# Kernel optimization log

Hardware: AMD Instinct MI355X
Metric: run time of the kernel (lower is better)

Reference implementation:

```python
import jax, jax.numpy as jnp
import numpy as np

N_ENTITY = 100000
D = 128          # entity_hidden_size = hidden_size // 2
HID = 256        # hidden_size
N_REL = 48
N_BASES = 8
N_EDGES = 1000000
B_SZ, E_LEN = 32, 32


def setup_inputs() -> dict:
    key = jax.random.key(0)
    ks = jax.random.split(key, 12)
    s = 0.05
    return {
        "node_embeds": jax.random.normal(ks[0], (N_ENTITY, D), jnp.float32) * s,
        "bases": jax.random.normal(ks[1], (N_BASES, D, D), jnp.float32) * s,
        "comp": jax.random.normal(ks[2], (N_REL, N_BASES), jnp.float32) * s,
        "root": jax.random.normal(ks[3], (D, D), jnp.float32) * s,
        "bias": jnp.zeros((D,), jnp.float32),
        "w1": jax.random.normal(ks[4], (D, D // 2), jnp.float32) * s,
        "b1": jnp.zeros((D // 2,), jnp.float32),
        "w2": jax.random.normal(ks[5], (D // 2, D), jnp.float32) * s,
        "b2": jnp.zeros((D,), jnp.float32),
        "wp": jax.random.normal(ks[6], (D, HID), jnp.float32) * s,
        "bp": jnp.zeros((HID,), jnp.float32),
        "edge_index": jax.random.randint(ks[7], (2, N_EDGES), 0, N_ENTITY, dtype=jnp.int32),
        "edge_type": jax.random.randint(ks[8], (N_EDGES,), 0, N_REL, dtype=jnp.int32),
        "entity_ids": jax.random.randint(ks[9], (B_SZ, E_LEN), 0, N_ENTITY, dtype=jnp.int32),
    }


def _rgcn(x, bases, comp, root, bias, edge_index, edge_type):
    # PyG RGCNConv with basis decomposition, aggr='mean' per (node, relation).
    n = x.shape[0]
    r, b = comp.shape
    src, dst = edge_index[0], edge_index[1]
    # per-(target, relation) in-degree for mean normalization
    seg = dst * r + edge_type                                   # [E]
    deg = jax.ops.segment_sum(jnp.ones_like(edge_type, jnp.float32), seg, num_segments=n * r)
    norm = 1.0 / jnp.maximum(deg, 1.0)
    c = comp[edge_type] * norm[seg][:, None]                    # [E, B] relation coeffs * norm
    x_src = x[src]                                              # [E, D] gather
    out = x @ root + bias                                       # root transform
    for k in range(b):                                          # small fixed basis loop
        agg = jax.ops.segment_sum(c[:, k:k + 1] * x_src, dst, num_segments=n)  # [N, D]
        out = out + agg @ bases[k]
    return out


def reference(node_embeds, bases, comp, root, bias, w1, b1, w2, b2, wp, bp,
              edge_index, edge_type, entity_ids):
    h = _rgcn(node_embeds, bases, comp, root, bias, edge_index, edge_type) + node_embeds
    h = (jax.nn.relu(h @ w1 + b1) @ w2 + b2) + h                # entity_proj1 + residual
    ent = h @ wp + bp                                           # entity_proj2 -> [N, HID]
    return ent[entity_ids]                                      # [B, L, HID]
```

## Files before the change

### kernel.cpp

```cpp
#include <hip/hip_runtime.h>

#define N_ENTITY 100000
#define D 128
#define HID 256
#define N_REL 48
#define N_BASES 8
#define N_EDGES 1000000
#define NPOS 1024
#define ECAP 96

#define OFF_MAP    0
#define OFF_BITMAP 100032
#define OFF_UCNT   103232
#define OFF_BKT    104256
#define OFF_ENT    202560

__global__ void k_register(const int* __restrict__ eids, int* __restrict__ map,
                           unsigned int* __restrict__ bitmap, int* __restrict__ ucnt) {
    int tid = threadIdx.x;
    for (int i = tid; i < 3200; i += 1024) bitmap[i] = 0u;
    ucnt[tid] = 0;
    __syncthreads();
    int e = eids[tid];
    atomicMin(&map[e], tid);
    atomicOr(&bitmap[e >> 5], 1u << (e & 31));
}

__global__ __launch_bounds__(256) void k_count(
        const int* __restrict__ src, const int* __restrict__ dst,
        const int* __restrict__ etype, const int* __restrict__ map,
        const unsigned int* __restrict__ bitmap, int* __restrict__ ucnt,
        int* __restrict__ bkt) {
    int base = (blockIdx.x * 256 + threadIdx.x) * 4;
    if (base >= N_EDGES) return;
    const int4 d4 = *reinterpret_cast<const int4*>(dst + base);
    #pragma unroll
    for (int q = 0; q < 4; ++q) {
        int d = (&d4.x)[q];
        if ((bitmap[d >> 5] >> (d & 31)) & 1u) {
            int e = base + q;
            int u = map[d];
            int pos = atomicAdd(&ucnt[u], 1);
            if (pos < ECAP)
                bkt[u * ECAP + pos] = src[e] | (etype[e] << 17);
        }
    }
}

__global__ __launch_bounds__(512) void k_fused2(
        const int* __restrict__ eids, const int* __restrict__ ucnt,
        const int* __restrict__ bkt, const float* __restrict__ x,
        const float* __restrict__ comp, const float* __restrict__ bases,
        const float* __restrict__ root, const float* __restrict__ bias,
        const float* __restrict__ w1, const float* __restrict__ b1,
        const float* __restrict__ w2, const float* __restrict__ b2,
        const float* __restrict__ wp, const float* __restrict__ bp,
        float* __restrict__ ent) {
    __shared__ float xs[2][D];
    __shared__ float accs[2][N_BASES * D];
    __shared__ float hs[2][D];
    __shared__ float t1s[2][D / 2];
    __shared__ float h2s[2][D];
    __shared__ float part[4096];
    __shared__ float ctab[ECAP][N_BASES];
    __shared__ int esrc[ECAP], eti[ECAP];
    __shared__ int deg48[N_REL];
    __shared__ int enames[2];

    int tid = threadIdx.x;
    int u0 = blockIdx.x * 2;
    if (tid < 2) enames[tid] = eids[u0 + tid];
    __syncthreads();
    if (tid < 256) {
        int s = tid >> 7, dd = tid & 127;
        xs[s][dd] = x[(size_t)enames[s] * D + dd];
    }

    {
        int d = tid & 127;
        int kg = tid >> 7;
        for (int s = 0; s < 2; ++s) {
            int u = u0 + s;
            int n = ucnt[u]; if (n > ECAP) n = ECAP;
            if (tid < N_REL) deg48[tid] = 0;
            if (tid < n) {
                int w = bkt[u * ECAP + tid];
                esrc[tid] = w & 0x1FFFF;
                eti[tid] = w >> 17;
            }
            __syncthreads();
            if (tid < n) atomicAdd(&deg48[eti[tid]], 1);
            __syncthreads();
            for (int ii = tid; ii < n * N_BASES; ii += 512) {
                int i = ii >> 3, k = ii & 7;
                int t = eti[i];
                ctab[i][k] = comp[t * N_BASES + k] / (float)max(deg48[t], 1);
            }
            __syncthreads();
            float a0 = 0.0f, a1 = 0.0f;
            #pragma unroll 4
            for (int i = 0; i < n; ++i) {
                float xv = x[(size_t)esrc[i] * D + d];
                a0 += ctab[i][2 * kg] * xv;
                a1 += ctab[i][2 * kg + 1] * xv;
            }
            accs[s][(2 * kg) * D + d] = a0;
            accs[s][(2 * kg + 1) * D + d] = a1;
            __syncthreads();
        }
    }

    {
        int jq = tid & 31, kc = tid >> 5;
        int j0 = jq * 4;
        float4 pA = {0, 0, 0, 0}, pB = {0, 0, 0, 0};
        #pragma unroll 8
        for (int ii = 0; ii < 8; ++ii) {
            int r = kc * 8 + ii;
            float4 w = *reinterpret_cast<const float4*>(root + r * D + j0);
            float aA = xs[0][r], aB = xs[1][r];
            pA.x += aA * w.x; pA.y += aA * w.y; pA.z += aA * w.z; pA.w += aA * w.w;
            pB.x += aB * w.x; pB.y += aB * w.y; pB.z += aB * w.z; pB.w += aB * w.w;
        }
        #pragma unroll 8
        for (int ii = 0; ii < 64; ++ii) {
            int r = kc * 64 + ii;
            float4 w = *reinterpret_cast<const float4*>(bases + (size_t)r * D + j0);
            float aA = accs[0][r], aB = accs[1][r];
            pA.x += aA * w.x; pA.y += aA * w.y; pA.z += aA * w.z; pA.w += aA * w.w;
            pB.x += aB * w.x; pB.y += aB * w.y; pB.z += aB * w.z; pB.w += aB * w.w;
        }
        float* p0 = part + kc * 256 + j0;
        p0[0] = pA.x; p0[1] = pA.y; p0[2] = pA.z; p0[3] = pA.w;
        float* p1 = p0 + 128;
        p1[0] = pB.x; p1[1] = pB.y; p1[2] = pB.z; p1[3] = pB.w;
    }
    __syncthreads();
    if (tid < 256) {
        int s = tid >> 7, j = tid & 127;
        float v = bias[j] + xs[s][j];
        #pragma unroll
        for (int q = 0; q < 16; ++q) v += part[q * 256 + s * 128 + j];
        hs[s][j] = v;
    }
    __syncthreads();

    {
        int oq = tid & 15, kc = tid >> 4;
        int o0 = oq * 4;
        float4 pA = {0, 0, 0, 0}, pB = {0, 0, 0, 0};
        #pragma unroll
        for (int ii = 0; ii < 4; ++ii) {
            int r = kc * 4 + ii;
            float4 w = *reinterpret_cast<const float4*>(w1 + r * (D / 2) + o0);
            float aA = hs[0][r], aB = hs[1][r];
            pA.x += aA * w.x; pA.y += aA * w.y; pA.z += aA * w.z; pA.w += aA * w.w;
            pB.x += aB * w.x; pB.y += aB * w.y; pB.z += aB * w.z; pB.w += aB * w.w;
        }
        float* p0 = part + kc * 128 + o0;
        p0[0] = pA.x; p0[1] = pA.y; p0[2] = pA.z; p0[3] = pA.w;
        float* p1 = p0 + 64;
        p1[0] = pB.x; p1[1] = pB.y; p1[2] = pB.z; p1[3] = pB.w;
    }
    __syncthreads();
    if (tid < 128) {
        int s = tid >> 6, o = tid & 63;
        float v = b1[o];
        #pragma unroll
        for (int q = 0; q < 32; ++q) v += part[q * 128 + s * 64 + o];
        t1s[s][o] = fmaxf(v, 0.0f);
    }
    __syncthreads();

    {
        int jq = tid & 31, kc = tid >> 5;
        int j0 = jq * 4;
        float4 pA = {0, 0, 0, 0}, pB = {0, 0, 0, 0};
        #pragma unroll
        for (int ii = 0; ii < 4; ++ii) {
            int r = kc * 4 + ii;
            float4 w = *reinterpret_cast<const float4*>(w2 + r * D + j0);
            float aA = t1s[0][r], aB = t1s[1][r];
            pA.x += aA * w.x; pA.y += aA * w.y; pA.z += aA * w.z; pA.w += aA * w.w;
            pB.x += aB * w.x; pB.y += aB * w.y; pB.z += aB * w.z; pB.w += aB * w.w;
        }
        float* p0 = part + kc * 256 + j0;
        p0[0] = pA.x; p0[1] = pA.y; p0[2] = pA.z; p0[3] = pA.w;
        float* p1 = p0 + 128;
        p1[0] = pB.x; p1[1] = pB.y; p1[2] = pB.z; p1[3] = pB.w;
    }
    __syncthreads();
    if (tid < 256) {
        int s = tid >> 7, j = tid & 127;
        float v = b2[j] + hs[s][j];
        #pragma unroll
        for (int q = 0; q < 16; ++q) v += part[q * 256 + s * 128 + j];
        h2s[s][j] = v;
    }
    __syncthreads();

    {
        int oq = tid & 63, kc = tid >> 6;
        int o0 = oq * 4;
        float4 pA = {0, 0, 0, 0}, pB = {0, 0, 0, 0};
        #pragma unroll 8
        for (int ii = 0; ii < 16; ++ii) {
            int r = kc * 16 + ii;
            float4 w = *reinterpret_cast<const float4*>(wp + r * HID + o0);
            float aA = h2s[0][r], aB = h2s[1][r];
            pA.x += aA * w.x; pA.y += aA * w.y; pA.z += aA * w.z; pA.w += aA * w.w;
            pB.x += aB * w.x; pB.y += aB * w.y; pB.z += aB * w.z; pB.w += aB * w.w;
        }
        float* p0 = part + kc * 512 + o0;
        p0[0] = pA.x; p0[1] = pA.y; p0[2] = pA.z; p0[3] = pA.w;
        float* p1 = p0 + 256;
        p1[0] = pB.x; p1[1] = pB.y; p1[2] = pB.z; p1[3] = pB.w;
    }
    __syncthreads();
    {
        int s = tid >> 8, o = tid & 255;
        float v = bp[o];
        #pragma unroll
        for (int q = 0; q < 8; ++q) v += part[q * 512 + s * 256 + o];
        ent[(size_t)(u0 + s) * HID + o] = v;
    }
}

__global__ void k_gather(const int* __restrict__ eids, const int* __restrict__ map,
                         const float* __restrict__ ent, float* __restrict__ out) {
    int pos = blockIdx.x;
    int u = map[eids[pos]];
    out[(size_t)pos * HID + threadIdx.x] = ent[(size_t)u * HID + threadIdx.x];
}

extern "C" void kernel_launch(void* const* d_in, const int* in_sizes, int n_in,
                              void* d_out, int out_size, void* d_ws, size_t ws_size,
                              hipStream_t stream) {
    const float* x     = (const float*)d_in[0];
    const float* bases = (const float*)d_in[1];
    const float* comp  = (const float*)d_in[2];
    const float* root  = (const float*)d_in[3];
    const float* bias  = (const float*)d_in[4];
    const float* w1    = (const float*)d_in[5];
    const float* b1    = (const float*)d_in[6];
    const float* w2    = (const float*)d_in[7];
    const float* b2    = (const float*)d_in[8];
    const float* wp    = (const float*)d_in[9];
    const float* bp    = (const float*)d_in[10];
    const int* eidx    = (const int*)d_in[11];
    const int* srcp    = eidx;
    const int* dstp    = eidx + N_EDGES;
    const int* etype   = (const int*)d_in[12];
    const int* eids    = (const int*)d_in[13];
    float* out = (float*)d_out;

    int* ws = (int*)d_ws;
    int* map            = ws + OFF_MAP;
    unsigned int* bmap  = (unsigned int*)(ws + OFF_BITMAP);
    int* ucnt           = ws + OFF_UCNT;
    int* bkt            = ws + OFF_BKT;
    float* ent          = (float*)(ws + OFF_ENT);

    hipMemsetAsync(map, 0x7F, (size_t)100032 * sizeof(int), stream);

    k_register<<<1, NPOS, 0, stream>>>(eids, map, bmap, ucnt);
    k_count<<<(N_EDGES / 4 + 255) / 256, 256, 0, stream>>>(srcp, dstp, etype, map,
                                                           bmap, ucnt, bkt);
    k_fused2<<<NPOS / 2, 512, 0, stream>>>(eids, ucnt, bkt, x, comp,
                                           bases, root, bias, w1, b1, w2, b2,
                                           wp, bp, ent);
    k_gather<<<NPOS, HID, 0, stream>>>(eids, map, ent, out);
}
```

Baseline: 146.5 us.

## Fuse whole pipeline into one cooperative kernel with grid syncs

Replaces the memset and the register, count, compute and gather kernels with a single cooperative launch of 256 blocks of 512 threads. Grid-wide syncs separate workspace init, entity registration and edge bucketing from the per-entity compute. The final gather is removed: each unique entity's output row is written straight to every position that references it, using per-entity position lists. Each block now handles four entities instead of two, which reuses each weight load across more rows but serialises more edge gathers per block and adds grid-sync overhead.

```diff
diff --git a/kernel.cpp b/kernel.cpp
--- a/kernel.cpp
+++ b/kernel.cpp
@@ -1,4 +1,7 @@
 #include <hip/hip_runtime.h>
+#include <hip/hip_cooperative_groups.h>
+
+namespace cg = cooperative_groups;
 
 #define N_ENTITY 100000
 #define D 128
@@ -8,70 +11,94 @@
 #define N_EDGES 1000000
 #define NPOS 1024
 #define ECAP 96
+#define PCAP 8
+#define GRIDSZ 256
+#define BLK 512
+#define NTHREADS (GRIDSZ * BLK)
 
 #define OFF_MAP    0
 #define OFF_BITMAP 100032
 #define OFF_UCNT   103232
-#define OFF_BKT    104256
-#define OFF_ENT    202560
-
-__global__ void k_register(const int* __restrict__ eids, int* __restrict__ map,
-                           unsigned int* __restrict__ bitmap, int* __restrict__ ucnt) {
+#define OFF_PCNT   104256
+#define OFF_PBUF   105280
+#define OFF_BKT    113472
+
+__global__ __launch_bounds__(BLK, 1) void k_mega(
+        const int* __restrict__ srcp, const int* __restrict__ dstp,
+        const int* __restrict__ etype, const int* __restrict__ eids,
+        const float* __restrict__ x, const float* __restrict__ comp,
+        const float* __restrict__ bases, const float* __restrict__ root,
+        const float* __restrict__ bias, const float* __restrict__ w1,
+        const float* __restrict__ b1, const float* __restrict__ w2,
+        const float* __restrict__ b2, const float* __restrict__ wp,
+        const float* __restrict__ bp, int* __restrict__ ws,
+        float* __restrict__ out) {
+    cg::grid_group grid = cg::this_grid();
+    int* map            = ws + OFF_MAP;
+    unsigned int* bmap  = (unsigned int*)(ws + OFF_BITMAP);
+    int* ucnt           = ws + OFF_UCNT;
+    int* pcnt           = ws + OFF_PCNT;
+    int* pbuf           = ws + OFF_PBUF;
+    int* bkt            = ws + OFF_BKT;
+
     int tid = threadIdx.x;
-    for (int i = tid; i < 3200; i += 1024) bitmap[i] = 0u;
-    ucnt[tid] = 0;
-    __syncthreads();
-    int e = eids[tid];
-    atomicMin(&map[e], tid);
-    atomicOr(&bitmap[e >> 5], 1u << (e & 31));
-}
-
-__global__ __launch_bounds__(256) void k_count(
-        const int* __restrict__ src, const int* __restrict__ dst,
-        const int* __restrict__ etype, const int* __restrict__ map,
-        const unsigned int* __restrict__ bitmap, int* __restrict__ ucnt,
-        int* __restrict__ bkt) {
-    int base = (blockIdx.x * 256 + threadIdx.x) * 4;
-    if (base >= N_EDGES) return;
-    const int4 d4 = *reinterpret_cast<const int4*>(dst + base);
-    #pragma unroll
-    for (int q = 0; q < 4; ++q) {
-        int d = (&d4.x)[q];
-        if ((bitmap[d >> 5] >> (d & 31)) & 1u) {
-            int e = base + q;
-            int u = map[d];
-            int pos = atomicAdd(&ucnt[u], 1);
-            if (pos < ECAP)
-                bkt[u * ECAP + pos] = src[e] | (etype[e] << 17);
-        }
-    }
-}
-
-__global__ __launch_bounds__(512) void k_fused2(
-        const int* __restrict__ eids, const int* __restrict__ ucnt,
-        const int* __restrict__ bkt, const float* __restrict__ x,
-        const float* __restrict__ comp, const float* __restrict__ bases,
-        const float* __restrict__ root, const float* __restrict__ bias,
-        const float* __restrict__ w1, const float* __restrict__ b1,
-        const float* __restrict__ w2, const float* __restrict__ b2,
-        const float* __restrict__ wp, const float* __restrict__ bp,
-        float* __restrict__ ent) {
-    __shared__ float xs[2][D];
-    __shared__ float accs[2][N_BASES * D];
-    __shared__ float hs[2][D];
-    __shared__ float t1s[2][D / 2];
-    __shared__ float h2s[2][D];
-    __shared__ float part[4096];
+    int gtid = blockIdx.x * BLK + tid;
+
+    for (int i = gtid; i < 105280; i += NTHREADS)
+        ws[i] = (i < 100032) ? 0x7F7F7F7F : 0;
+    grid.sync();
+
+    if (gtid < NPOS) {
+        int e = eids[gtid];
+        atomicMin(&map[e], gtid);
+        atomicOr(&bmap[e >> 5], 1u << (e & 31));
+    }
+    grid.sync();
+
+    if (gtid < NPOS) {
+        int u = map[eids[gtid]];
+        int q = atomicAdd(&pcnt[u], 1);
+        if (q < PCAP) pbuf[u * PCAP + q] = gtid;
+    }
+    for (int b = gtid; b < N_EDGES / 4; b += NTHREADS) {
+        const int4 d4 = *reinterpret_cast<const int4*>(dstp + b * 4);
+        #pragma unroll
+        for (int q = 0; q < 4; ++q) {
+            int d = (&d4.x)[q];
+            if ((bmap[d >> 5] >> (d & 31)) & 1u) {
+                int e = b * 4 + q;
+                int u = map[d];
+                int pos = atomicAdd(&ucnt[u], 1);
+                if (pos < ECAP)
+                    bkt[u * ECAP + pos] = srcp[e] | (etype[e] << 17);
+            }
+        }
+    }
+    grid.sync();
+
+    __shared__ float xs[4][D];
+    __shared__ float accs[4][N_BASES * D];
+    __shared__ float hs[4][D];
+    __shared__ float t1s[4][D / 2];
+    __shared__ float h2s[4][D];
+    __shared__ float part[8192];
     __shared__ float ctab[ECAP][N_BASES];
     __shared__ int esrc[ECAP], eti[ECAP];
     __shared__ int deg48[N_REL];
-    __shared__ int enames[2];
-
-    int tid = threadIdx.x;
-    int u0 = blockIdx.x * 2;
-    if (tid < 2) enames[tid] = eids[u0 + tid];
-    __syncthreads();
-    if (tid < 256) {
+    __shared__ int enames[4], npos4[4], plist4[4][PCAP];
+
+    int u0 = blockIdx.x * 4;
+    if (tid < 4) {
+        enames[tid] = eids[u0 + tid];
+        int np = pcnt[u0 + tid];
+        npos4[tid] = np < PCAP ? np : PCAP;
+    }
+    if (tid < 4 * PCAP) {
+        int s = tid >> 3, q = tid & (PCAP - 1);
+        plist4[s][q] = pbuf[(u0 + s) * PCAP + q];
+    }
+    __syncthreads();
+    {
         int s = tid >> 7, dd = tid & 127;
         xs[s][dd] = x[(size_t)enames[s] * D + dd];
     }
@@ -79,7 +106,7 @@
     {
         int d = tid & 127;
         int kg = tid >> 7;
-        for (int s = 0; s < 2; ++s) {
+        for (int s = 0; s < 4; ++s) {
             int u = u0 + s;
             int n = ucnt[u]; if (n > ECAP) n = ECAP;
             if (tid < N_REL) deg48[tid] = 0;
@@ -91,7 +118,7 @@
             __syncthreads();
             if (tid < n) atomicAdd(&deg48[eti[tid]], 1);
             __syncthreads();
-            for (int ii = tid; ii < n * N_BASES; ii += 512) {
+            for (int ii = tid; ii < n * N_BASES; ii += BLK) {
                 int i = ii >> 3, k = ii & 7;
                 int t = eti[i];
                 ctab[i][k] = comp[t * N_BASES + k] / (float)max(deg48[t], 1);
@@ -113,34 +140,39 @@
     {
         int jq = tid & 31, kc = tid >> 5;
         int j0 = jq * 4;
-        float4 pA = {0, 0, 0, 0}, pB = {0, 0, 0, 0};
+        float4 p0 = {0,0,0,0}, p1 = {0,0,0,0}, p2 = {0,0,0,0}, p3 = {0,0,0,0};
         #pragma unroll 8
         for (int ii = 0; ii < 8; ++ii) {
             int r = kc * 8 + ii;
             float4 w = *reinterpret_cast<const float4*>(root + r * D + j0);
-            float aA = xs[0][r], aB = xs[1][r];
-            pA.x += aA * w.x; pA.y += aA * w.y; pA.z += aA * w.z; pA.w += aA * w.w;
-            pB.x += aB * w.x; pB.y += aB * w.y; pB.z += aB * w.z; pB.w += aB * w.w;
+            float a0 = xs[0][r], a1 = xs[1][r], a2 = xs[2][r], a3 = xs[3][r];
+            p0.x += a0*w.x; p0.y += a0*w.y; p0.z += a0*w.z; p0.w += a0*w.w;
+            p1.x += a1*w.x; p1.y += a1*w.y; p1.z += a1*w.z; p1.w += a1*w.w;
+            p2.x += a2*w.x; p2.y += a2*w.y; p2.z += a2*w.z; p2.w += a2*w.w;
+            p3.x += a3*w.x; p3.y += a3*w.y; p3.z += a3*w.z; p3.w += a3*w.w;
         }
         #pragma unroll 8
         for (int ii = 0; ii < 64; ++ii) {
             int r = kc * 64 + ii;
             float4 w = *reinterpret_cast<const float4*>(bases + (size_t)r * D + j0);
-            float aA = accs[0][r], aB = accs[1][r];
-            pA.x += aA * w.x; pA.y += aA * w.y; pA.z += aA * w.z; pA.w += aA * w.w;
-            pB.x += aB * w.x; pB.y += aB * w.y; pB.z += aB * w.z; pB.w += aB * w.w;
-        }
-        float* p0 = part + kc * 256 + j0;
-        p0[0] = pA.x; p0[1] = pA.y; p0[2] = pA.z; p0[3] = pA.w;
-        float* p1 = p0 + 128;
-        p1[0] = pB.x; p1[1] = pB.y; p1[2] = pB.z; p1[3] = pB.w;
-    }
-    __syncthreads();
-    if (tid < 256) {
+            float a0 = accs[0][r], a1 = accs[1][r], a2 = accs[2][r], a3 = accs[3][r];
+            p0.x += a0*w.x; p0.y += a0*w.y; p0.z += a0*w.z; p0.w += a0*w.w;
+            p1.x += a1*w.x; p1.y += a1*w.y; p1.z += a1*w.z; p1.w += a1*w.w;
+            p2.x += a2*w.x; p2.y += a2*w.y; p2.z += a2*w.z; p2.w += a2*w.w;
+            p3.x += a3*w.x; p3.y += a3*w.y; p3.z += a3*w.z; p3.w += a3*w.w;
+        }
+        float* pp = part + kc * 512 + j0;
+        pp[0]=p0.x; pp[1]=p0.y; pp[2]=p0.z; pp[3]=p0.w;  pp += 128;
+        pp[0]=p1.x; pp[1]=p1.y; pp[2]=p1.z; pp[3]=p1.w;  pp += 128;
+        pp[0]=p2.x; pp[1]=p2.y; pp[2]=p2.z; pp[3]=p2.w;  pp += 128;
+        pp[0]=p3.x; pp[1]=p3.y; pp[2]=p3.z; pp[3]=p3.w;
+    }
+    __syncthreads();
+    {
         int s = tid >> 7, j = tid & 127;
         float v = bias[j] + xs[s][j];
         #pragma unroll
-        for (int q = 0; q < 16; ++q) v += part[q * 256 + s * 128 + j];
+        for (int q = 0; q < 16; ++q) v += part[q * 512 + s * 128 + j];
         hs[s][j] = v;
     }
     __syncthreads();
@@ -148,26 +180,29 @@
     {
         int oq = tid & 15, kc = tid >> 4;
         int o0 = oq * 4;
-        float4 pA = {0, 0, 0, 0}, pB = {0, 0, 0, 0};
+        float4 p0 = {0,0,0,0}, p1 = {0,0,0,0}, p2 = {0,0,0,0}, p3 = {0,0,0,0};
         #pragma unroll
         for (int ii = 0; ii < 4; ++ii) {
             int r = kc * 4 + ii;
             float4 w = *reinterpret_cast<const float4*>(w1 + r * (D / 2) + o0);
-            float aA = hs[0][r], aB = hs[1][r];
-            pA.x += aA * w.x; pA.y += aA * w.y; pA.z += aA * w.z; pA.w += aA * w.w;
-            pB.x += aB * w.x; pB.y += aB * w.y; pB.z += aB * w.z; pB.w += aB * w.w;
-        }
-        float* p0 = part + kc * 128 + o0;
-        p0[0] = pA.x; p0[1] = pA.y; p0[2] = pA.z; p0[3] = pA.w;
-        float* p1 = p0 + 64;
-        p1[0] = pB.x; p1[1] = pB.y; p1[2] = pB.z; p1[3] = pB.w;
-    }
-    __syncthreads();
-    if (tid < 128) {
+            float a0 = hs[0][r], a1 = hs[1][r], a2 = hs[2][r], a3 = hs[3][r];
+            p0.x += a0*w.x; p0.y += a0*w.y; p0.z += a0*w.z; p0.w += a0*w.w;
+            p1.x += a1*w.x; p1.y += a1*w.y; p1.z += a1*w.z; p1.w += a1*w.w;
+            p2.x += a2*w.x; p2.y += a2*w.y; p2.z += a2*w.z; p2.w += a2*w.w;
+            p3.x += a3*w.x; p3.y += a3*w.y; p3.z += a3*w.z; p3.w += a3*w.w;
+        }
+        float* pp = part + kc * 256 + o0;
+        pp[0]=p0.x; pp[1]=p0.y; pp[2]=p0.z; pp[3]=p0.w;  pp += 64;
+        pp[0]=p1.x; pp[1]=p1.y; pp[2]=p1.z; pp[3]=p1.w;  pp += 64;
+        pp[0]=p2.x; pp[1]=p2.y; pp[2]=p2.z; pp[3]=p2.w;  pp += 64;
+        pp[0]=p3.x; pp[1]=p3.y; pp[2]=p3.z; pp[3]=p3.w;
+    }
+    __syncthreads();
+    if (tid < 256) {
         int s = tid >> 6, o = tid & 63;
         float v = b1[o];
         #pragma unroll
-        for (int q = 0; q < 32; ++q) v += part[q * 128 + s * 64 + o];
+        for (int q = 0; q < 32; ++q) v += part[q * 256 + s * 64 + o];
         t1s[s][o] = fmaxf(v, 0.0f);
     }
     __syncthreads();
@@ -175,26 +210,29 @@
     {
         int jq = tid & 31, kc = tid >> 5;
         int j0 = jq * 4;
-        float4 pA = {0, 0, 0, 0}, pB = {0, 0, 0, 0};
+        float4 p0 = {0,0,0,0}, p1 = {0,0,0,0}, p2 = {0,0,0,0}, p3 = {0,0,0,0};
         #pragma unroll
         for (int ii = 0; ii < 4; ++ii) {
             int r = kc * 4 + ii;
             float4 w = *reinterpret_cast<const float4*>(w2 + r * D + j0);
-            float aA = t1s[0][r], aB = t1s[1][r];
-            pA.x += aA * w.x; pA.y += aA * w.y; pA.z += aA * w.z; pA.w += aA * w.w;
-            pB.x += aB * w.x; pB.y += aB * w.y; pB.z += aB * w.z; pB.w += aB * w.w;
-        }
-        float* p0 = part + kc * 256 + j0;
-        p0[0] = pA.x; p0[1] = pA.y; p0[2] = pA.z; p0[3] = pA.w;
-        float* p1 = p0 + 128;
-        p1[0] = pB.x; p1[1] = pB.y; p1[2] = pB.z; p1[3] = pB.w;
-    }
-    __syncthreads();
-    if (tid < 256) {
+            float a0 = t1s[0][r], a1 = t1s[1][r], a2 = t1s[2][r], a3 = t1s[3][r];
+            p0.x += a0*w.x; p0.y += a0*w.y; p0.z += a0*w.z; p0.w += a0*w.w;
+            p1.x += a1*w.x; p1.y += a1*w.y; p1.z += a1*w.z; p1.w += a1*w.w;
+            p2.x += a2*w.x; p2.y += a2*w.y; p2.z += a2*w.z; p2.w += a2*w.w;
+            p3.x += a3*w.x; p3.y += a3*w.y; p3.z += a3*w.z; p3.w += a3*w.w;
+        }
+        float* pp = part + kc * 512 + j0;
+        pp[0]=p0.x; pp[1]=p0.y; pp[2]=p0.z; pp[3]=p0.w;  pp += 128;
+        pp[0]=p1.x; pp[1]=p1.y; pp[2]=p1.z; pp[3]=p1.w;  pp += 128;
+        pp[0]=p2.x; pp[1]=p2.y; pp[2]=p2.z; pp[3]=p2.w;  pp += 128;
+        pp[0]=p3.x; pp[1]=p3.y; pp[2]=p3.z; pp[3]=p3.w;
+    }
+    __syncthreads();
+    {
         int s = tid >> 7, j = tid & 127;
         float v = b2[j] + hs[s][j];
         #pragma unroll
-        for (int q = 0; q < 16; ++q) v += part[q * 256 + s * 128 + j];
+        for (int q = 0; q < 16; ++q) v += part[q * 512 + s * 128 + j];
         h2s[s][j] = v;
     }
     __syncthreads();
@@ -202,35 +240,35 @@
     {
         int oq = tid & 63, kc = tid >> 6;
         int o0 = oq * 4;
-        float4 pA = {0, 0, 0, 0}, pB = {0, 0, 0, 0};
+        float4 p0 = {0,0,0,0}, p1 = {0,0,0,0}, p2 = {0,0,0,0}, p3 = {0,0,0,0};
         #pragma unroll 8
         for (int ii = 0; ii < 16; ++ii) {
             int r = kc * 16 + ii;
             float4 w = *reinterpret_cast<const float4*>(wp + r * HID + o0);
-            float aA = h2s[0][r], aB = h2s[1][r];
-            pA.x += aA * w.x; pA.y += aA * w.y; pA.z += aA * w.z; pA.w += aA * w.w;
-            pB.x += aB * w.x; pB.y += aB * w.y; pB.z += aB * w.z; pB.w += aB * w.w;
-        }
-        float* p0 = part + kc * 512 + o0;
-        p0[0] = pA.x; p0[1] = pA.y; p0[2] = pA.z; p0[3] = pA.w;
-        float* p1 = p0 + 256;
-        p1[0] = pB.x; p1[1] = pB.y; p1[2] = pB.z; p1[3] = pB.w;
-    }
-    __syncthreads();
-    {
-        int s = tid >> 8, o = tid & 255;
-        float v = bp[o];
-        #pragma unroll
-        for (int q = 0; q < 8; ++q) v += part[q * 512 + s * 256 + o];
-        ent[(size_t)(u0 + s) * HID + o] = v;
-    }
-}
-
-__global__ void k_gather(const int* __restrict__ eids, const int* __restrict__ map,
-                         const float* __restrict__ ent, float* __restrict__ out) {
-    int pos = blockIdx.x;
-    int u = map[eids[pos]];
-    out[(size_t)pos * HID + threadIdx.x] = ent[(size_t)u * HID + threadIdx.x];
+            float a0 = h2s[0][r], a1 = h2s[1][r], a2 = h2s[2][r], a3 = h2s[3][r];
+            p0.x += a0*w.x; p0.y += a0*w.y; p0.z += a0*w.z; p0.w += a0*w.w;
+            p1.x += a1*w.x; p1.y += a1*w.y; p1.z += a1*w.z; p1.w += a1*w.w;
+            p2.x += a2*w.x; p2.y += a2*w.y; p2.z += a2*w.z; p2.w += a2*w.w;
+            p3.x += a3*w.x; p3.y += a3*w.y; p3.z += a3*w.z; p3.w += a3*w.w;
+        }
+        float* pp = part + kc * 1024 + o0;
+        pp[0]=p0.x; pp[1]=p0.y; pp[2]=p0.z; pp[3]=p0.w;  pp += 256;
+        pp[0]=p1.x; pp[1]=p1.y; pp[2]=p1.z; pp[3]=p1.w;  pp += 256;
+        pp[0]=p2.x; pp[1]=p2.y; pp[2]=p2.z; pp[3]=p2.w;  pp += 256;
+        pp[0]=p3.x; pp[1]=p3.y; pp[2]=p3.z; pp[3]=p3.w;
+    }
+    __syncthreads();
+    {
+        int o = tid & 255;
+        for (int s = tid >> 8; s < 4; s += 2) {
+            float v = bp[o];
+            #pragma unroll
+            for (int q = 0; q < 8; ++q) v += part[q * 1024 + s * 256 + o];
+            int np = npos4[s];
+            for (int pi = 0; pi < np; ++pi)
+                out[(size_t)plist4[s][pi] * HID + o] = v;
+        }
+    }
 }
 
 extern "C" void kernel_launch(void* const* d_in, const int* in_sizes, int n_in,
@@ -253,21 +291,14 @@
     const int* etype   = (const int*)d_in[12];
     const int* eids    = (const int*)d_in[13];
     float* out = (float*)d_out;
-
     int* ws = (int*)d_ws;
-    int* map            = ws + OFF_MAP;
-    unsigned int* bmap  = (unsigned int*)(ws + OFF_BITMAP);
-    int* ucnt           = ws + OFF_UCNT;
-    int* bkt            = ws + OFF_BKT;
-    float* ent          = (float*)(ws + OFF_ENT);
-
-    hipMemsetAsync(map, 0x7F, (size_t)100032 * sizeof(int), stream);
-
-    k_register<<<1, NPOS, 0, stream>>>(eids, map, bmap, ucnt);
-    k_count<<<(N_EDGES / 4 + 255) / 256, 256, 0, stream>>>(srcp, dstp, etype, map,
-                                                           bmap, ucnt, bkt);
-    k_fused2<<<NPOS / 2, 512, 0, stream>>>(eids, ucnt, bkt, x, comp,
-                                           bases, root, bias, w1, b1, w2, b2,
-                                           wp, bp, ent);
-    k_gather<<<NPOS, HID, 0, stream>>>(eids, map, ent, out);
+
+    void* args[] = {
+        (void*)&srcp, (void*)&dstp, (void*)&etype, (void*)&eids,
+        (void*)&x, (void*)&comp, (void*)&bases, (void*)&root,
+        (void*)&bias, (void*)&w1, (void*)&b1, (void*)&w2,
+        (void*)&b2, (void*)&wp, (void*)&bp, (void*)&ws, (void*)&out
+    };
+    hipLaunchCooperativeKernel((void*)k_mega, dim3(GRIDSZ), dim3(BLK),
+                               args, 0, stream);
 }
```

New measurement: 238.4 us. 1.63x slower.

## Process four entities per block and scatter outputs directly, dropping gather kernel

Applied to the files above, without the earlier changes.

The fused kernel now handles four unique entities per block instead of two, so each weight row loaded from global memory is reused across four rows. Neighbour aggregation for all four entities runs in parallel, with 8 basis accumulators per thread instead of looping over entities. A position list built in the register kernel lets the fused kernel write results straight to the output positions, removing the intermediate entity buffer and the separate gather launch. In exchange there are half as many blocks (256), which may lower occupancy and parallelism on a large GPU, and more registers per thread.

```diff
diff --git a/kernel.cpp b/kernel.cpp
--- a/kernel.cpp
+++ b/kernel.cpp
@@ -8,22 +8,30 @@
 #define N_EDGES 1000000
 #define NPOS 1024
 #define ECAP 96
+#define PCAP 16
 
 #define OFF_MAP    0
 #define OFF_BITMAP 100032
 #define OFF_UCNT   103232
-#define OFF_BKT    104256
-#define OFF_ENT    202560
+#define OFF_PCNT   104256
+#define OFF_PBUF   105280
+#define OFF_BKT    121664
 
 __global__ void k_register(const int* __restrict__ eids, int* __restrict__ map,
-                           unsigned int* __restrict__ bitmap, int* __restrict__ ucnt) {
+                           unsigned int* __restrict__ bitmap, int* __restrict__ ucnt,
+                           int* __restrict__ pcnt, int* __restrict__ pbuf) {
     int tid = threadIdx.x;
     for (int i = tid; i < 3200; i += 1024) bitmap[i] = 0u;
     ucnt[tid] = 0;
+    pcnt[tid] = 0;
     __syncthreads();
     int e = eids[tid];
     atomicMin(&map[e], tid);
     atomicOr(&bitmap[e >> 5], 1u << (e & 31));
+    __syncthreads();
+    int u = map[e];
+    int q = atomicAdd(&pcnt[u], 1);
+    if (q < PCAP) pbuf[u * PCAP + q] = tid;
 }
 
 __global__ __launch_bounds__(256) void k_count(
@@ -47,190 +55,202 @@
     }
 }
 
-__global__ __launch_bounds__(512) void k_fused2(
+__global__ __launch_bounds__(512) void k_fused(
         const int* __restrict__ eids, const int* __restrict__ ucnt,
+        const int* __restrict__ pcnt, const int* __restrict__ pbuf,
         const int* __restrict__ bkt, const float* __restrict__ x,
         const float* __restrict__ comp, const float* __restrict__ bases,
         const float* __restrict__ root, const float* __restrict__ bias,
         const float* __restrict__ w1, const float* __restrict__ b1,
         const float* __restrict__ w2, const float* __restrict__ b2,
         const float* __restrict__ wp, const float* __restrict__ bp,
-        float* __restrict__ ent) {
-    __shared__ float xs[2][D];
-    __shared__ float accs[2][N_BASES * D];
-    __shared__ float hs[2][D];
-    __shared__ float t1s[2][D / 2];
-    __shared__ float h2s[2][D];
-    __shared__ float part[4096];
-    __shared__ float ctab[ECAP][N_BASES];
-    __shared__ int esrc[ECAP], eti[ECAP];
-    __shared__ int deg48[N_REL];
-    __shared__ int enames[2];
+        float* __restrict__ out) {
+    __shared__ float smem[8192];
+    __shared__ float hs4[4 * 128];
+    __shared__ float t1s4[4 * 64];
+    __shared__ float h2s4[4 * 128];
+    __shared__ float comp_s[N_REL * N_BASES];
+    __shared__ int deg4[4 * N_REL];
+    __shared__ int esrc4[4][ECAP], eti4[4][ECAP];
+    __shared__ int enames4[4], ncnt4[4], npos4[4], plist4[4][PCAP];
 
     int tid = threadIdx.x;
-    int u0 = blockIdx.x * 2;
-    if (tid < 2) enames[tid] = eids[u0 + tid];
-    __syncthreads();
-    if (tid < 256) {
-        int s = tid >> 7, dd = tid & 127;
-        xs[s][dd] = x[(size_t)enames[s] * D + dd];
-    }
-
-    {
-        int d = tid & 127;
-        int kg = tid >> 7;
-        for (int s = 0; s < 2; ++s) {
-            int u = u0 + s;
-            int n = ucnt[u]; if (n > ECAP) n = ECAP;
-            if (tid < N_REL) deg48[tid] = 0;
-            if (tid < n) {
-                int w = bkt[u * ECAP + tid];
-                esrc[tid] = w & 0x1FFFF;
-                eti[tid] = w >> 17;
-            }
-            __syncthreads();
-            if (tid < n) atomicAdd(&deg48[eti[tid]], 1);
-            __syncthreads();
-            for (int ii = tid; ii < n * N_BASES; ii += 512) {
-                int i = ii >> 3, k = ii & 7;
-                int t = eti[i];
-                ctab[i][k] = comp[t * N_BASES + k] / (float)max(deg48[t], 1);
-            }
-            __syncthreads();
-            float a0 = 0.0f, a1 = 0.0f;
-            #pragma unroll 4
-            for (int i = 0; i < n; ++i) {
-                float xv = x[(size_t)esrc[i] * D + d];
-                a0 += ctab[i][2 * kg] * xv;
-                a1 += ctab[i][2 * kg + 1] * xv;
-            }
-            accs[s][(2 * kg) * D + d] = a0;
-            accs[s][(2 * kg + 1) * D + d] = a1;
-            __syncthreads();
-        }
-    }
+    int u0 = blockIdx.x * 4;
+
+    if (tid < 4) {
+        enames4[tid] = eids[u0 + tid];
+        int c = ucnt[u0 + tid];  ncnt4[tid] = c < ECAP ? c : ECAP;
+        int p = pcnt[u0 + tid];  npos4[tid] = p < PCAP ? p : PCAP;
+    }
+    if (tid < 4 * PCAP) {
+        int s = tid >> 4, q = tid & (PCAP - 1);
+        plist4[s][q] = pbuf[(u0 + s) * PCAP + q];
+    }
+    if (tid < N_REL * N_BASES) comp_s[tid] = comp[tid];
+    if (tid < 4 * N_REL) deg4[tid] = 0;
+    __syncthreads();
+
+    {
+        int s = tid >> 7, i = tid & 127;
+        if (i < ncnt4[s]) {
+            int w = bkt[(u0 + s) * ECAP + i];
+            esrc4[s][i] = w & 0x1FFFF;
+            eti4[s][i] = w >> 17;
+        }
+        smem[s * 1152 + i] = x[(size_t)enames4[s] * D + i];
+    }
+    __syncthreads();
+    if (tid < 4 * ECAP) {
+        int s = tid / ECAP, i = tid - s * ECAP;
+        if (i < ncnt4[s]) atomicAdd(&deg4[s * N_REL + eti4[s][i]], 1);
+    }
+    __syncthreads();
+    {
+        int dd = tid & 127, s = tid >> 7;
+        float a[8] = {0, 0, 0, 0, 0, 0, 0, 0};
+        int n = ncnt4[s];
+        #pragma unroll 4
+        for (int i = 0; i < n; ++i) {
+            int t = eti4[s][i];
+            float rn = 1.0f / (float)max(deg4[s * N_REL + t], 1);
+            float xv = x[(size_t)esrc4[s][i] * D + dd];
+            #pragma unroll
+            for (int k = 0; k < 8; ++k) a[k] += comp_s[t * 8 + k] * rn * xv;
+        }
+        #pragma unroll
+        for (int k = 0; k < 8; ++k)
+            smem[s * 1152 + 128 + k * 128 + dd] = a[k];
+    }
+    __syncthreads();
 
     {
         int jq = tid & 31, kc = tid >> 5;
         int j0 = jq * 4;
-        float4 pA = {0, 0, 0, 0}, pB = {0, 0, 0, 0};
-        #pragma unroll 8
-        for (int ii = 0; ii < 8; ++ii) {
-            int r = kc * 8 + ii;
-            float4 w = *reinterpret_cast<const float4*>(root + r * D + j0);
-            float aA = xs[0][r], aB = xs[1][r];
-            pA.x += aA * w.x; pA.y += aA * w.y; pA.z += aA * w.z; pA.w += aA * w.w;
-            pB.x += aB * w.x; pB.y += aB * w.y; pB.z += aB * w.z; pB.w += aB * w.w;
-        }
-        #pragma unroll 8
-        for (int ii = 0; ii < 64; ++ii) {
-            int r = kc * 64 + ii;
-            float4 w = *reinterpret_cast<const float4*>(bases + (size_t)r * D + j0);
-            float aA = accs[0][r], aB = accs[1][r];
-            pA.x += aA * w.x; pA.y += aA * w.y; pA.z += aA * w.z; pA.w += aA * w.w;
-            pB.x += aB * w.x; pB.y += aB * w.y; pB.z += aB * w.z; pB.w += aB * w.w;
-        }
-        float* p0 = part + kc * 256 + j0;
-        p0[0] = pA.x; p0[1] = pA.y; p0[2] = pA.z; p0[3] = pA.w;
-        float* p1 = p0 + 128;
-        p1[0] = pB.x; p1[1] = pB.y; p1[2] = pB.z; p1[3] = pB.w;
-    }
-    __syncthreads();
-    if (tid < 256) {
+        float4 p0 = {0,0,0,0}, p1 = {0,0,0,0}, p2 = {0,0,0,0}, p3 = {0,0,0,0};
+        int r0 = kc * 72;
+        #pragma unroll 4
+        for (int ii = 0; ii < 72; ++ii) {
+            int r = r0 + ii;
+            const float* wrow = (r < 128) ? (root + (size_t)r * D)
+                                          : (bases + (size_t)(r - 128) * D);
+            float4 w = *reinterpret_cast<const float4*>(wrow + j0);
+            float a0 = smem[0 * 1152 + r], a1 = smem[1 * 1152 + r];
+            float a2 = smem[2 * 1152 + r], a3 = smem[3 * 1152 + r];
+            p0.x += a0*w.x; p0.y += a0*w.y; p0.z += a0*w.z; p0.w += a0*w.w;
+            p1.x += a1*w.x; p1.y += a1*w.y; p1.z += a1*w.z; p1.w += a1*w.w;
+            p2.x += a2*w.x; p2.y += a2*w.y; p2.z += a2*w.z; p2.w += a2*w.w;
+            p3.x += a3*w.x; p3.y += a3*w.y; p3.z += a3*w.z; p3.w += a3*w.w;
+        }
+        __syncthreads();
+        *reinterpret_cast<float4*>(&smem[kc * 512 +   0 + j0]) = p0;
+        *reinterpret_cast<float4*>(&smem[kc * 512 + 128 + j0]) = p1;
+        *reinterpret_cast<float4*>(&smem[kc * 512 + 256 + j0]) = p2;
+        *reinterpret_cast<float4*>(&smem[kc * 512 + 384 + j0]) = p3;
+    }
+    __syncthreads();
+    {
         int s = tid >> 7, j = tid & 127;
-        float v = bias[j] + xs[s][j];
-        #pragma unroll
-        for (int q = 0; q < 16; ++q) v += part[q * 256 + s * 128 + j];
-        hs[s][j] = v;
+        float v = bias[j] + x[(size_t)enames4[s] * D + j];
+        #pragma unroll
+        for (int q = 0; q < 16; ++q) v += smem[q * 512 + s * 128 + j];
+        hs4[s * 128 + j] = v;
     }
     __syncthreads();
 
     {
         int oq = tid & 15, kc = tid >> 4;
         int o0 = oq * 4;
-        float4 pA = {0, 0, 0, 0}, pB = {0, 0, 0, 0};
+        float4 p0 = {0,0,0,0}, p1 = {0,0,0,0}, p2 = {0,0,0,0}, p3 = {0,0,0,0};
         #pragma unroll
         for (int ii = 0; ii < 4; ++ii) {
             int r = kc * 4 + ii;
-            float4 w = *reinterpret_cast<const float4*>(w1 + r * (D / 2) + o0);
-            float aA = hs[0][r], aB = hs[1][r];
-            pA.x += aA * w.x; pA.y += aA * w.y; pA.z += aA * w.z; pA.w += aA * w.w;
-            pB.x += aB * w.x; pB.y += aB * w.y; pB.z += aB * w.z; pB.w += aB * w.w;
-        }
-        float* p0 = part + kc * 128 + o0;
-        p0[0] = pA.x; p0[1] = pA.y; p0[2] = pA.z; p0[3] = pA.w;
-        float* p1 = p0 + 64;
-        p1[0] = pB.x; p1[1] = pB.y; p1[2] = pB.z; p1[3] = pB.w;
-    }
-    __syncthreads();
-    if (tid < 128) {
+            float4 w = *reinterpret_cast<const float4*>(w1 + (size_t)r * (D/2) + o0);
+            float a0 = hs4[0*128 + r], a1 = hs4[1*128 + r];
+            float a2 = hs4[2*128 + r], a3 = hs4[3*128 + r];
+            p0.x += a0*w.x; p0.y += a0*w.y; p0.z += a0*w.z; p0.w += a0*w.w;
+            p1.x += a1*w.x; p1.y += a1*w.y; p1.z += a1*w.z; p1.w += a1*w.w;
+            p2.x += a2*w.x; p2.y += a2*w.y; p2.z += a2*w.z; p2.w += a2*w.w;
+            p3.x += a3*w.x; p3.y += a3*w.y; p3.z += a3*w.z; p3.w += a3*w.w;
+        }
+        *reinterpret_cast<float4*>(&smem[kc * 256 +   0 + o0]) = p0;
+        *reinterpret_cast<float4*>(&smem[kc * 256 +  64 + o0]) = p1;
+        *reinterpret_cast<float4*>(&smem[kc * 256 + 128 + o0]) = p2;
+        *reinterpret_cast<float4*>(&smem[kc * 256 + 192 + o0]) = p3;
+    }
+    __syncthreads();
+    if (tid < 256) {
         int s = tid >> 6, o = tid & 63;
         float v = b1[o];
         #pragma unroll
-        for (int q = 0; q < 32; ++q) v += part[q * 128 + s * 64 + o];
-        t1s[s][o] = fmaxf(v, 0.0f);
+        for (int q = 0; q < 32; ++q) v += smem[q * 256 + s * 64 + o];
+        t1s4[s * 64 + o] = fmaxf(v, 0.0f);
     }
     __syncthreads();
 
     {
         int jq = tid & 31, kc = tid >> 5;
         int j0 = jq * 4;
-        float4 pA = {0, 0, 0, 0}, pB = {0, 0, 0, 0};
+        float4 p0 = {0,0,0,0}, p1 = {0,0,0,0}, p2 = {0,0,0,0}, p3 = {0,0,0,0};
         #pragma unroll
         for (int ii = 0; ii < 4; ++ii) {
             int r = kc * 4 + ii;
-            float4 w = *reinterpret_cast<const float4*>(w2 + r * D + j0);
-            float aA = t1s[0][r], aB = t1s[1][r];
-            pA.x += aA * w.x; pA.y += aA * w.y; pA.z += aA * w.z; pA.w += aA * w.w;
-            pB.x += aB * w.x; pB.y += aB * w.y; pB.z += aB * w.z; pB.w += aB * w.w;
-        }
-        float* p0 = part + kc * 256 + j0;
-        p0[0] = pA.x; p0[1] = pA.y; p0[2] = pA.z; p0[3] = pA.w;
-        float* p1 = p0 + 128;
-        p1[0] = pB.x; p1[1] = pB.y; p1[2] = pB.z; p1[3] = pB.w;
-    }
-    __syncthreads();
-    if (tid < 256) {
+            float4 w = *reinterpret_cast<const float4*>(w2 + (size_t)r * D + j0);
+            float a0 = t1s4[0*64 + r], a1 = t1s4[1*64 + r];
+            float a2 = t1s4[2*64 + r], a3 = t1s4[3*64 + r];
+            p0.x += a0*w.x; p0.y += a0*w.y; p0.z += a0*w.z; p0.w += a0*w.w;
+            p1.x += a1*w.x; p1.y += a1*w.y; p1.z += a1*w.z; p1.w += a1*w.w;
+            p2.x += a2*w.x; p2.y += a2*w.y; p2.z += a2*w.z; p2.w += a2*w.w;
+            p3.x += a3*w.x; p3.y += a3*w.y; p3.z += a3*w.z; p3.w += a3*w.w;
+        }
+        *reinterpret_cast<float4*>(&smem[kc * 512 +   0 + j0]) = p0;
+        *reinterpret_cast<float4*>(&smem[kc * 512 + 128 + j0]) = p1;
+        *reinterpret_cast<float4*>(&smem[kc * 512 + 256 + j0]) = p2;
+        *reinterpret_cast<float4*>(&smem[kc * 512 + 384 + j0]) = p3;
+    }
+    __syncthreads();
+    {
         int s = tid >> 7, j = tid & 127;
-        float v = b2[j] + hs[s][j];
-        #pragma unroll
-        for (int q = 0; q < 16; ++q) v += part[q * 256 + s * 128 + j];
-        h2s[s][j] = v;
+        float v = b2[j] + hs4[s * 128 + j];
+        #pragma unroll
+        for (int q = 0; q < 16; ++q) v += smem[q * 512 + s * 128 + j];
+        h2s4[s * 128 + j] = v;
     }
     __syncthreads();
 
     {
         int oq = tid & 63, kc = tid >> 6;
         int o0 = oq * 4;
-        float4 pA = {0, 0, 0, 0}, pB = {0, 0, 0, 0};
+        float4 p0 = {0,0,0,0}, p1 = {0,0,0,0}, p2 = {0,0,0,0}, p3 = {0,0,0,0};
         #pragma unroll 8
         for (int ii = 0; ii < 16; ++ii) {
             int r = kc * 16 + ii;
-            float4 w = *reinterpret_cast<const float4*>(wp + r * HID + o0);
-            float aA = h2s[0][r], aB = h2s[1][r];
-            pA.x += aA * w.x; pA.y += aA * w.y; pA.z += aA * w.z; pA.w += aA * w.w;
-            pB.x += aB * w.x; pB.y += aB * w.y; pB.z += aB * w.z; pB.w += aB * w.w;
-        }
-        float* p0 = part + kc * 512 + o0;
-        p0[0] = pA.x; p0[1] = pA.y; p0[2] = pA.z; p0[3] = pA.w;
-        float* p1 = p0 + 256;
-        p1[0] = pB.x; p1[1] = pB.y; p1[2] = pB.z; p1[3] = pB.w;
-    }
-    __syncthreads();
-    {
-        int s = tid >> 8, o = tid & 255;
-        float v = bp[o];
-        #pragma unroll
-        for (int q = 0; q < 8; ++q) v += part[q * 512 + s * 256 + o];
-        ent[(size_t)(u0 + s) * HID + o] = v;
-    }
-}
-
-__global__ void k_gather(const int* __restrict__ eids, const int* __restrict__ map,
-                         const float* __restrict__ ent, float* __restrict__ out) {
-    int pos = blockIdx.x;
-    int u = map[eids[pos]];
-    out[(size_t)pos * HID + threadIdx.x] = ent[(size_t)u * HID + threadIdx.x];
+            float4 w = *reinterpret_cast<const float4*>(wp + (size_t)r * HID + o0);
+            float a0 = h2s4[0*128 + r], a1 = h2s4[1*128 + r];
+            float a2 = h2s4[2*128 + r], a3 = h2s4[3*128 + r];
+            p0.x += a0*w.x; p0.y += a0*w.y; p0.z += a0*w.z; p0.w += a0*w.w;
+            p1.x += a1*w.x; p1.y += a1*w.y; p1.z += a1*w.z; p1.w += a1*w.w;
+            p2.x += a2*w.x; p2.y += a2*w.y; p2.z += a2*w.z; p2.w += a2*w.w;
+            p3.x += a3*w.x; p3.y += a3*w.y; p3.z += a3*w.z; p3.w += a3*w.w;
+        }
+        *reinterpret_cast<float4*>(&smem[kc * 1024 +   0 + o0]) = p0;
+        *reinterpret_cast<float4*>(&smem[kc * 1024 + 256 + o0]) = p1;
+        *reinterpret_cast<float4*>(&smem[kc * 1024 + 512 + o0]) = p2;
+        *reinterpret_cast<float4*>(&smem[kc * 1024 + 768 + o0]) = p3;
+    }
+    __syncthreads();
+    {
+        int o = tid & 255, sb = tid >> 8;
+        #pragma unroll
+        for (int si = 0; si < 2; ++si) {
+            int s = sb + si * 2;
+            float v = bp[o];
+            #pragma unroll
+            for (int q = 0; q < 8; ++q) v += smem[q * 1024 + s * 256 + o];
+            int np = npos4[s];
+            for (int pi = 0; pi < np; ++pi)
+                out[(size_t)plist4[s][pi] * HID + o] = v;
+        }
+    }
 }
 
 extern "C" void kernel_launch(void* const* d_in, const int* in_sizes, int n_in,
@@ -258,16 +278,16 @@
     int* map            = ws + OFF_MAP;
     unsigned int* bmap  = (unsigned int*)(ws + OFF_BITMAP);
     int* ucnt           = ws + OFF_UCNT;
+    int* pcnt           = ws + OFF_PCNT;
+    int* pbuf           = ws + OFF_PBUF;
     int* bkt            = ws + OFF_BKT;
-    float* ent          = (float*)(ws + OFF_ENT);
 
     hipMemsetAsync(map, 0x7F, (size_t)100032 * sizeof(int), stream);
 
-    k_register<<<1, NPOS, 0, stream>>>(eids, map, bmap, ucnt);
+    k_register<<<1, NPOS, 0, stream>>>(eids, map, bmap, ucnt, pcnt, pbuf);
     k_count<<<(N_EDGES / 4 + 255) / 256, 256, 0, stream>>>(srcp, dstp, etype, map,
                                                            bmap, ucnt, bkt);
-    k_fused2<<<NPOS / 2, 512, 0, stream>>>(eids, ucnt, bkt, x, comp,
-                                           bases, root, bias, w1, b1, w2, b2,
-                                           wp, bp, ent);
-    k_gather<<<NPOS, HID, 0, stream>>>(eids, map, ent, out);
-}
+    k_fused<<<NPOS / 4, 512, 0, stream>>>(eids, ucnt, pcnt, pbuf, bkt, x, comp,
+                                          bases, root, bias, w1, b1, w2, b2,
+                                          wp, bp, out);
+}
```

Result: faster. 140.7 us (-3.9%).
